# Kernel tuning notes

Hardware: AMD Instinct MI355X
Metric: run time of the kernel (lower is better)

## Reference

```python
import jax, jax.numpy as jnp
import numpy as np
from functools import partial

B, F, H, G, S = 8192, 16, 128, 4, 20  # batch, features, hidden, goals, SUBSTEPS
A_IZH, B_IZH, C_IZH, D_IZH = 0.02, 0.2, -65.0, 8.0  # Izhikevich 'RS' params
RATE_DECAY = 0.9
GAMMA, LR = 0.95, 1e-3


def izh_step(v, u, rate, I):
    """One Izhikevich substep (dt=1): returns new (v, u, rate, spike)."""
    v_new = v + (0.04 * v * v + 5.0 * v + 140.0 - u + I)
    u_new = u + A_IZH * (B_IZH * v - u)
    spike = (v_new >= 30.0).astype(v.dtype)
    v_new = jnp.where(spike > 0, C_IZH, v_new)
    u_new = u_new + spike * D_IZH
    rate_new = RATE_DECAY * rate + (1.0 - RATE_DECAY) * spike
    return v_new, u_new, rate_new, spike


def build_features(energy, threat, food_visible, goal, cls_probs, DA_, NA_):
    # [B,16] = [4 scalars | one-hot goal (4) | cls_probs (5) | DA | NA | hunger]
    base = jnp.stack([energy / 100.0, threat, food_visible, 1.0 - energy / 100.0], axis=-1)
    onehot = jax.nn.one_hot(goal, G, dtype=base.dtype)
    tail = jnp.stack([DA_, NA_, jnp.maximum(0.0, 0.5 - energy / 100.0)], axis=-1)
    return jnp.concatenate([base, onehot, cls_probs, tail], axis=-1)


def setup_inputs() -> dict:
    key = jax.random.key(0)
    ks = jax.random.split(key, 16)
    energy = jax.random.uniform(ks[0], (B,)) * 100.0
    threat = jax.random.uniform(ks[1], (B,))
    food_visible = jax.random.uniform(ks[2], (B,))
    goal = jax.random.randint(ks[3], (B,), 0, G)
    prev_goal = jax.random.randint(ks[4], (B,), 0, G)
    DA_ = jax.random.uniform(ks[5], (B,))
    NA_ = jax.random.uniform(ks[6], (B,))
    reward = jax.random.normal(ks[7], (B,)) * 0.5
    cls_probs = jax.nn.softmax(jax.random.normal(ks[8], (B, 5)), axis=-1)
    a_in = 0.5 * np.sqrt(6.0 / (F + H))   # xavier_uniform gain 0.5
    a_out = 0.3 * np.sqrt(6.0 / (H + G))  # xavier_uniform gain 0.3
    W_in_w = jax.random.uniform(ks[9], (B, H, F), minval=-a_in, maxval=a_in)
    W_in_b = jax.random.uniform(ks[10], (B, H), minval=-1.0, maxval=1.0) / np.sqrt(F)
    W_out_w = jax.random.uniform(ks[11], (B, G, H), minval=-a_out, maxval=a_out)
    W_out_b = jax.random.uniform(ks[12], (B, G), minval=-1.0, maxval=1.0) / np.sqrt(H)
    hv = jnp.full((B, H), -65.0)
    hu = B_IZH * hv
    hrate = jnp.zeros((B, H))
    vv = jnp.full((B, G), -65.0)
    vu = B_IZH * vv
    vrate = jnp.zeros((B, G))
    elig_in = jnp.zeros((B, H, F))
    elig_out = jnp.zeros((B, G, H))
    prev_values = jnp.zeros((B, G))
    prev_features = jax.random.uniform(ks[13], (B, F))
    noise = jax.random.normal(ks[14], (S, B, H))
    return dict(energy=energy, threat=threat, food_visible=food_visible, goal=goal,
                prev_goal=prev_goal, DA_=DA_, NA_=NA_, reward=reward, cls_probs=cls_probs,
                W_in_w=W_in_w, W_in_b=W_in_b, W_out_w=W_out_w, W_out_b=W_out_b,
                hv=hv, hu=hu, hrate=hrate, vv=vv, vu=vu, vrate=vrate,
                elig_in=elig_in, elig_out=elig_out, prev_values=prev_values,
                prev_features=prev_features, noise=noise)


def reference(energy, threat, food_visible, goal, prev_goal, DA_, NA_, reward, cls_probs,
              W_in_w, W_in_b, W_out_w, W_out_b, hv, hu, hrate, vv, vu, vrate,
              elig_in, elig_out, prev_values, prev_features, noise):
    features = build_features(energy, threat, food_visible, goal, cls_probs, DA_, NA_)  # [B,F]
    I_in = jnp.einsum('bhf,bf->bh', W_in_w, features) + W_in_b
    I_in = I_in * (5.0 / (jnp.mean(jnp.abs(I_in), axis=-1, keepdims=True) + 1e-8))

    def step(carry, nz):
        hv, hu, hrate, vv, vu, vrate, hsp, vsp = carry
        hv, hu, hrate, sp_h = izh_step(hv, hu, hrate, I_in + 0.3 * nz)
        I_out = jnp.einsum('bgh,bh->bg', W_out_w, hrate) + W_out_b
        I_out = I_out * (4.0 / (jnp.mean(jnp.abs(I_out), axis=-1, keepdims=True) + 1e-8))
        vv, vu, vrate, sp_v = izh_step(vv, vu, vrate, I_out)
        return (hv, hu, hrate, vv, vu, vrate, hsp + sp_h, vsp + sp_v), None

    carry0 = (hv, hu, hrate, vv, vu, vrate, jnp.zeros_like(hrate), jnp.zeros_like(vrate))
    (hv, hu, hrate, vv, vu, vrate, h_spikes, v_spikes), _ = jax.lax.scan(step, carry0, noise)

    values = jnp.einsum('bgh,bh->bg', W_out_w, hrate) + W_out_b  # [B,G]
    V_now = jnp.take_along_axis(values, goal[:, None], axis=1)[:, 0]
    V_prev = jnp.take_along_axis(prev_values, prev_goal[:, None], axis=1)[:, 0]
    td = reward + GAMMA * V_now - V_prev  # [B]

    elig_in_new = 0.9 * elig_in + hrate[:, :, None] * prev_features[:, None, :]
    elig_out_new = 0.9 * elig_out + vrate[:, :, None] * hrate[:, None, :]

    upd = (jnp.abs(td) > 1e-3)  # [B]
    scale = (LR * td * DA_)[:, None, None]
    W_in_new = jnp.where(upd[:, None, None], jnp.clip(W_in_w + scale * elig_in_new, -3.0, 3.0), W_in_w)
    W_out_new = jnp.where(upd[:, None, None], jnp.clip(W_out_w + scale * elig_out_new, -3.0, 3.0), W_out_w)

    hidden_active = jnp.mean((h_spikes > 0).astype(values.dtype), axis=-1)  # [B]
    return values, td, hidden_active, W_in_new, W_out_new, elig_in_new, elig_out_new
```

## Files before the change

### kernel.cpp

```cpp
#include <hip/hip_runtime.h>


namespace {

constexpr int F = 16;
constexpr int H = 128;
constexpr int G = 4;
constexpr int S = 20;

__device__ __forceinline__ float clip3(float x) {
    return fminf(fmaxf(x, -3.0f), 3.0f);
}

__global__ __launch_bounds__(64)
void spiking_critic_kernel(
    const float* __restrict__ energy,
    const float* __restrict__ threat,
    const float* __restrict__ food_visible,
    const int*   __restrict__ goal,
    const int*   __restrict__ prev_goal,
    const float* __restrict__ DA,
    const float* __restrict__ NA,
    const float* __restrict__ reward,
    const float* __restrict__ cls_probs,
    const float* __restrict__ W_in_w,
    const float* __restrict__ W_in_b,
    const float* __restrict__ W_out_w,
    const float* __restrict__ W_out_b,
    const float* __restrict__ hv_in,
    const float* __restrict__ hu_in,
    const float* __restrict__ hrate_in,
    const float* __restrict__ vv_in,
    const float* __restrict__ vu_in,
    const float* __restrict__ vrate_in,
    const float* __restrict__ elig_in,
    const float* __restrict__ elig_out,
    const float* __restrict__ prev_values,
    const float* __restrict__ prev_features,
    const float* __restrict__ noise,
    float* __restrict__ out_values,
    float* __restrict__ out_td,
    float* __restrict__ out_hidden,
    float* __restrict__ out_Win,
    float* __restrict__ out_Wout,
    float* __restrict__ out_ein,
    float* __restrict__ out_eout,
    int nB)
{
    const int b = blockIdx.x;
    const int t = threadIdx.x;

    __shared__ __align__(16) float w_in_lds[H * F];
    __shared__ __align__(16) float w_out_lds[G * H];
    __shared__ __align__(16) float hrate_lds[H];
    __shared__ __align__(16) float feat[F];
    __shared__ __align__(16) float pf_lds[F];

    const float4* wi4 = (const float4*)(W_in_w + (size_t)b * (H * F));
    float4* wl4 = (float4*)w_in_lds;
    #pragma unroll
    for (int k = 0; k < 8; ++k) wl4[t + 64 * k] = wi4[t + 64 * k];
    const float4* wog = (const float4*)(W_out_w + (size_t)b * (G * H));
    float4* wo4 = (float4*)w_out_lds;
    #pragma unroll
    for (int k = 0; k < 2; ++k) wo4[t + 64 * k] = wog[t + 64 * k];

    if (t < F) pf_lds[t] = prev_features[(size_t)b * F + t];

    if (t < F) {
        float e = energy[b];
        float v;
        if      (t == 0)  v = e / 100.0f;
        else if (t == 1)  v = threat[b];
        else if (t == 2)  v = food_visible[b];
        else if (t == 3)  v = 1.0f - e / 100.0f;
        else if (t < 8)   v = (goal[b] == (t - 4)) ? 1.0f : 0.0f;
        else if (t < 13)  v = cls_probs[(size_t)b * 5 + (t - 8)];
        else if (t == 13) v = DA[b];
        else if (t == 14) v = NA[b];
        else              v = fmaxf(0.0f, 0.5f - e / 100.0f);
        feat[t] = v;
    }
    __syncthreads();

    float Iraw0 = W_in_b[(size_t)b * H + t];
    float Iraw1 = W_in_b[(size_t)b * H + t + 64];
    #pragma unroll
    for (int j = 0; j < 4; ++j) {
        float4 w0 = ((const float4*)w_in_lds)[t * 4 + j];
        float4 w1 = ((const float4*)w_in_lds)[(t + 64) * 4 + j];
        float fx = feat[4 * j + 0], fy = feat[4 * j + 1];
        float fz = feat[4 * j + 2], fw = feat[4 * j + 3];
        Iraw0 += w0.x * fx + w0.y * fy + w0.z * fz + w0.w * fw;
        Iraw1 += w1.x * fx + w1.y * fy + w1.z * fz + w1.w * fw;
    }
    float a = fabsf(Iraw0) + fabsf(Iraw1);
    #pragma unroll
    for (int m = 32; m >= 1; m >>= 1) a += __shfl_xor(a, m, 64);
    float inorm = 5.0f / (a * (1.0f / 128.0f) + 1e-8f);
    float Iin0 = Iraw0 * inorm;
    float Iin1 = Iraw1 * inorm;

    float wc0[G], wc1[G], wob[G];
    #pragma unroll
    for (int g = 0; g < G; ++g) {
        wc0[g] = w_out_lds[g * H + t];
        wc1[g] = w_out_lds[g * H + t + 64];
        wob[g] = W_out_b[(size_t)b * G + g];
    }

    float hv0 = hv_in[(size_t)b * H + t],      hv1 = hv_in[(size_t)b * H + t + 64];
    float hu0 = hu_in[(size_t)b * H + t],      hu1 = hu_in[(size_t)b * H + t + 64];
    float hr0 = hrate_in[(size_t)b * H + t],   hr1 = hrate_in[(size_t)b * H + t + 64];
    float vv[G], vu[G], vr[G];
    #pragma unroll
    for (int g = 0; g < G; ++g) {
        vv[g] = vv_in[(size_t)b * G + g];
        vu[g] = vu_in[(size_t)b * G + g];
        vr[g] = vrate_in[(size_t)b * G + g];
    }

    float nz0[S], nz1[S];
    #pragma unroll
    for (int s = 0; s < S; ++s) {
        nz0[s] = noise[((size_t)s * nB + b) * H + t];
        nz1[s] = noise[((size_t)s * nB + b) * H + t + 64];
    }

    float hsp0 = 0.0f, hsp1 = 0.0f;
    float vals[G] = {0.f, 0.f, 0.f, 0.f};

    #pragma unroll
    for (int s = 0; s < S; ++s) {
        {
            float I  = Iin0 + 0.3f * nz0[s];
            float vn = hv0 + (0.04f * hv0 * hv0 + 5.0f * hv0 + 140.0f - hu0 + I);
            float un = hu0 + 0.02f * (0.2f * hv0 - hu0);
            float sp = (vn >= 30.0f) ? 1.0f : 0.0f;
            hv0 = (sp > 0.0f) ? -65.0f : vn;
            hu0 = un + sp * 8.0f;
            hr0 = 0.9f * hr0 + 0.1f * sp;
            hsp0 += sp;
        }
        {
            float I  = Iin1 + 0.3f * nz1[s];
            float vn = hv1 + (0.04f * hv1 * hv1 + 5.0f * hv1 + 140.0f - hu1 + I);
            float un = hu1 + 0.02f * (0.2f * hv1 - hu1);
            float sp = (vn >= 30.0f) ? 1.0f : 0.0f;
            hv1 = (sp > 0.0f) ? -65.0f : vn;
            hu1 = un + sp * 8.0f;
            hr1 = 0.9f * hr1 + 0.1f * sp;
            hsp1 += sp;
        }

        float p0 = wc0[0] * hr0 + wc1[0] * hr1;
        float p1 = wc0[1] * hr0 + wc1[1] * hr1;
        float p2 = wc0[2] * hr0 + wc1[2] * hr1;
        float p3 = wc0[3] * hr0 + wc1[3] * hr1;
        #pragma unroll
        for (int m = 32; m >= 1; m >>= 1) {
            p0 += __shfl_xor(p0, m, 64);
            p1 += __shfl_xor(p1, m, 64);
            p2 += __shfl_xor(p2, m, 64);
            p3 += __shfl_xor(p3, m, 64);
        }
        vals[0] = p0 + wob[0];
        vals[1] = p1 + wob[1];
        vals[2] = p2 + wob[2];
        vals[3] = p3 + wob[3];

        float m4 = 0.25f * (fabsf(vals[0]) + fabsf(vals[1])
                          + fabsf(vals[2]) + fabsf(vals[3]));
        float onorm = 4.0f / (m4 + 1e-8f);
        #pragma unroll
        for (int g = 0; g < G; ++g) {
            float Io = vals[g] * onorm;
            float vn = vv[g] + (0.04f * vv[g] * vv[g] + 5.0f * vv[g] + 140.0f - vu[g] + Io);
            float un = vu[g] + 0.02f * (0.2f * vv[g] - vu[g]);
            float sp = (vn >= 30.0f) ? 1.0f : 0.0f;
            vv[g] = (sp > 0.0f) ? -65.0f : vn;
            vu[g] = un + sp * 8.0f;
            vr[g] = 0.9f * vr[g] + 0.1f * sp;
        }
    }

    hrate_lds[t] = hr0;
    hrate_lds[t + 64] = hr1;
    __syncthreads();

    if (t < G) {
        float v = (t == 0) ? vals[0] : (t == 1) ? vals[1] : (t == 2) ? vals[2] : vals[3];
        out_values[(size_t)b * G + t] = v;
    }

    unsigned long long mb0 = __ballot(hsp0 > 0.0f);
    unsigned long long mb1 = __ballot(hsp1 > 0.0f);
    float hidden = (float)(__popcll(mb0) + __popcll(mb1)) * (1.0f / 128.0f);

    int gl = goal[b];
    float Vnow  = (gl == 0) ? vals[0] : (gl == 1) ? vals[1] : (gl == 2) ? vals[2] : vals[3];
    float Vprev = prev_values[(size_t)b * G + prev_goal[b]];
    float td = reward[b] + 0.95f * Vnow - Vprev;
    if (t == 0) {
        out_td[b]     = td;
        out_hidden[b] = hidden;
    }

    const float scale = 1e-3f * td * DA[b];
    const bool  upd   = fabsf(td) > 1e-3f;

    {
        const float4* ei4 = (const float4*)(elig_in + (size_t)b * (H * F));
        float4* oW = (float4*)(out_Win + (size_t)b * (H * F));
        float4* oE = (float4*)(out_ein + (size_t)b * (H * F));
        float4 pf = ((const float4*)pf_lds)[t & 3];
        #pragma unroll
        for (int k = 0; k < 8; ++k) {
            int q = t + 64 * k;
            float4 e  = ei4[q];
            float  hrv = hrate_lds[q >> 2];
            float4 en;
            en.x = 0.9f * e.x + hrv * pf.x;
            en.y = 0.9f * e.y + hrv * pf.y;
            en.z = 0.9f * e.z + hrv * pf.z;
            en.w = 0.9f * e.w + hrv * pf.w;
            oE[q] = en;
            float4 w = wl4[q];
            float4 wn;
            if (upd) {
                wn.x = clip3(w.x + scale * en.x);
                wn.y = clip3(w.y + scale * en.y);
                wn.z = clip3(w.z + scale * en.z);
                wn.w = clip3(w.w + scale * en.w);
            } else {
                wn = w;
            }
            oW[q] = wn;
        }
    }

    {
        const float4* eo4 = (const float4*)(elig_out + (size_t)b * (G * H));
        float4* oW = (float4*)(out_Wout + (size_t)b * (G * H));
        float4* oE = (float4*)(out_eout + (size_t)b * (G * H));
        #pragma unroll
        for (int k = 0; k < 2; ++k) {
            int q  = t + 64 * k;
            int gg = q >> 5;
            float vrv = (gg == 0) ? vr[0] : (gg == 1) ? vr[1] : (gg == 2) ? vr[2] : vr[3];
            float4 hq = ((const float4*)hrate_lds)[q & 31];
            float4 e  = eo4[q];
            float4 en;
            en.x = 0.9f * e.x + vrv * hq.x;
            en.y = 0.9f * e.y + vrv * hq.y;
            en.z = 0.9f * e.z + vrv * hq.z;
            en.w = 0.9f * e.w + vrv * hq.w;
            oE[q] = en;
            float4 w = ((const float4*)w_out_lds)[q];
            float4 wn;
            if (upd) {
                wn.x = clip3(w.x + scale * en.x);
                wn.y = clip3(w.y + scale * en.y);
                wn.z = clip3(w.z + scale * en.z);
                wn.w = clip3(w.w + scale * en.w);
            } else {
                wn = w;
            }
            oW[q] = wn;
        }
    }
}

}

extern "C" void kernel_launch(void* const* d_in, const int* in_sizes, int n_in,
                              void* d_out, int out_size, void* d_ws, size_t ws_size,
                              hipStream_t stream) {
    const int nB = in_sizes[0];

    float* out        = (float*)d_out;
    float* out_values = out;
    float* out_td     = out_values + (size_t)nB * G;
    float* out_hidden = out_td + nB;
    float* out_Win    = out_hidden + nB;
    float* out_Wout   = out_Win + (size_t)nB * H * F;
    float* out_ein    = out_Wout + (size_t)nB * G * H;
    float* out_eout   = out_ein + (size_t)nB * H * F;

    spiking_critic_kernel<<<dim3(nB), dim3(64), 0, stream>>>(
        (const float*)d_in[0],  (const float*)d_in[1],  (const float*)d_in[2],
        (const int*)  d_in[3],  (const int*)  d_in[4],
        (const float*)d_in[5],  (const float*)d_in[6],  (const float*)d_in[7],
        (const float*)d_in[8],  (const float*)d_in[9],  (const float*)d_in[10],
        (const float*)d_in[11], (const float*)d_in[12], (const float*)d_in[13],
        (const float*)d_in[14], (const float*)d_in[15], (const float*)d_in[16],
        (const float*)d_in[17], (const float*)d_in[18], (const float*)d_in[19],
        (const float*)d_in[20], (const float*)d_in[21], (const float*)d_in[22],
        (const float*)d_in[23],
        out_values, out_td, out_hidden, out_Win, out_Wout, out_ein, out_eout,
        nB);
}
```

Measured before the change: 412.5 us.

## Drop LDS staging, pack four batches per block, stream noise and use nontemporal stores

Removes all shared memory. The input-projection matvec now runs straight from global float4 loads, with a quad shuffle reduction and a permuted hidden-unit mapping. Hidden rates are exchanged through wave shuffles instead of LDS. Each 256-thread block now handles four batch rows, one wave each, with launch bounds raised for occupancy. The 20-entry noise register arrays become a two-deep prefetch ring. Outputs are written with nontemporal stores and weights are re-read from global rather than cached. All of this aims to cut LDS use, syncthreads and register pressure so more waves can hide memory latency, at the cost of re-reading the weights and doing extra shuffle work.

```diff
diff --git a/kernel.cpp b/kernel.cpp
--- a/kernel.cpp
+++ b/kernel.cpp
@@ -8,11 +8,26 @@
 constexpr int G = 4;
 constexpr int S = 20;
 
+typedef float vfloat4 __attribute__((ext_vector_type(4)));
+
 __device__ __forceinline__ float clip3(float x) {
     return fminf(fmaxf(x, -3.0f), 3.0f);
 }
 
-__global__ __launch_bounds__(64)
+__device__ __forceinline__ void nt_store4(float4 v, float4* p) {
+    vfloat4 x = {v.x, v.y, v.z, v.w};
+    __builtin_nontemporal_store(x, (vfloat4*)p);
+}
+
+__device__ __forceinline__ float hrate_at(int h, float hr0, float hr1) {
+    int m   = h >> 4;
+    int src = ((h & 15) << 2) | (m >> 1);
+    float a = __shfl(hr0, src, 64);
+    float b = __shfl(hr1, src, 64);
+    return (m & 1) ? b : a;
+}
+
+__global__ __launch_bounds__(256, 7)
 void spiking_critic_kernel(
     const float* __restrict__ energy,
     const float* __restrict__ threat,
@@ -47,93 +62,100 @@
     float* __restrict__ out_eout,
     int nB)
 {
-    const int b = blockIdx.x;
-    const int t = threadIdx.x;
-
-    __shared__ __align__(16) float w_in_lds[H * F];
-    __shared__ __align__(16) float w_out_lds[G * H];
-    __shared__ __align__(16) float hrate_lds[H];
-    __shared__ __align__(16) float feat[F];
-    __shared__ __align__(16) float pf_lds[F];
+    const int t = threadIdx.x & 63;
+    int b = blockIdx.x * 4 + (threadIdx.x >> 6);
+    b = __builtin_amdgcn_readfirstlane(b);
+    if (b >= nB) return;
+
+    const int j = t & 3;
+
+    const float e_b   = energy[b];
+    const float thr_b = threat[b];
+    const float fv_b  = food_visible[b];
+    const int   gl_b  = goal[b];
+    const float da_b  = DA[b];
+    const float na_b  = NA[b];
+    const float c0 = cls_probs[(size_t)b * 5 + 0];
+    const float c1 = cls_probs[(size_t)b * 5 + 1];
+    const float c2 = cls_probs[(size_t)b * 5 + 2];
+    const float c3 = cls_probs[(size_t)b * 5 + 3];
+    const float c4 = cls_probs[(size_t)b * 5 + 4];
+    const float en100 = e_b / 100.0f;
+
+    const float g0 = (gl_b == 0) ? 1.0f : 0.0f;
+    const float g1 = (gl_b == 1) ? 1.0f : 0.0f;
+    const float g2 = (gl_b == 2) ? 1.0f : 0.0f;
+    const float g3 = (gl_b == 3) ? 1.0f : 0.0f;
+    const float hunger = fmaxf(0.0f, 0.5f - en100);
+
+    const bool j1 = (j & 1) != 0;
+    const bool j2 = (j & 2) != 0;
+    float fx = j2 ? (j1 ? c4     : c0) : (j1 ? g0 : en100);
+    float fy = j2 ? (j1 ? da_b   : c1) : (j1 ? g1 : thr_b);
+    float fz = j2 ? (j1 ? na_b   : c2) : (j1 ? g2 : fv_b);
+    float fw = j2 ? (j1 ? hunger : c3) : (j1 ? g3 : 1.0f - en100);
 
     const float4* wi4 = (const float4*)(W_in_w + (size_t)b * (H * F));
-    float4* wl4 = (float4*)w_in_lds;
-    #pragma unroll
-    for (int k = 0; k < 8; ++k) wl4[t + 64 * k] = wi4[t + 64 * k];
-    const float4* wog = (const float4*)(W_out_w + (size_t)b * (G * H));
-    float4* wo4 = (float4*)w_out_lds;
-    #pragma unroll
-    for (int k = 0; k < 2; ++k) wo4[t + 64 * k] = wog[t + 64 * k];
-
-    if (t < F) pf_lds[t] = prev_features[(size_t)b * F + t];
-
-    if (t < F) {
-        float e = energy[b];
-        float v;
-        if      (t == 0)  v = e / 100.0f;
-        else if (t == 1)  v = threat[b];
-        else if (t == 2)  v = food_visible[b];
-        else if (t == 3)  v = 1.0f - e / 100.0f;
-        else if (t < 8)   v = (goal[b] == (t - 4)) ? 1.0f : 0.0f;
-        else if (t < 13)  v = cls_probs[(size_t)b * 5 + (t - 8)];
-        else if (t == 13) v = DA[b];
-        else if (t == 14) v = NA[b];
-        else              v = fmaxf(0.0f, 0.5f - e / 100.0f);
-        feat[t] = v;
-    }
-    __syncthreads();
-
-    float Iraw0 = W_in_b[(size_t)b * H + t];
-    float Iraw1 = W_in_b[(size_t)b * H + t + 64];
-    #pragma unroll
-    for (int j = 0; j < 4; ++j) {
-        float4 w0 = ((const float4*)w_in_lds)[t * 4 + j];
-        float4 w1 = ((const float4*)w_in_lds)[(t + 64) * 4 + j];
-        float fx = feat[4 * j + 0], fy = feat[4 * j + 1];
-        float fz = feat[4 * j + 2], fw = feat[4 * j + 3];
-        Iraw0 += w0.x * fx + w0.y * fy + w0.z * fz + w0.w * fw;
-        Iraw1 += w1.x * fx + w1.y * fy + w1.z * fz + w1.w * fw;
-    }
+    float p[8];
+    #pragma unroll
+    for (int k = 0; k < 8; ++k) {
+        float4 w = wi4[t + 64 * k];
+        p[k] = w.x * fx + w.y * fy + w.z * fz + w.w * fw;
+    }
+    #pragma unroll
+    for (int k = 0; k < 8; ++k) {
+        p[k] += __shfl_xor(p[k], 1, 64);
+        p[k] += __shfl_xor(p[k], 2, 64);
+        p[k] += W_in_b[(size_t)b * H + (t >> 2) + 16 * k];
+    }
+    const int h0 = (t >> 2) + 32 * j;
+    const int h1 = h0 + 16;
+    float Ir0a = j1 ? p[2] : p[0], Ir0b = j1 ? p[6] : p[4];
+    float Iraw0 = j2 ? Ir0b : Ir0a;
+    float Ir1a = j1 ? p[3] : p[1], Ir1b = j1 ? p[7] : p[5];
+    float Iraw1 = j2 ? Ir1b : Ir1a;
+
     float a = fabsf(Iraw0) + fabsf(Iraw1);
     #pragma unroll
     for (int m = 32; m >= 1; m >>= 1) a += __shfl_xor(a, m, 64);
-    float inorm = 5.0f / (a * (1.0f / 128.0f) + 1e-8f);
-    float Iin0 = Iraw0 * inorm;
-    float Iin1 = Iraw1 * inorm;
-
-    float wc0[G], wc1[G], wob[G];
+    const float inorm = 5.0f / (a * (1.0f / 128.0f) + 1e-8f);
+    const float Iin0 = Iraw0 * inorm;
+    const float Iin1 = Iraw1 * inorm;
+
+    float wc0[G], wc1[G], wob[G], vv[G], vu[G], vr[G];
     #pragma unroll
     for (int g = 0; g < G; ++g) {
-        wc0[g] = w_out_lds[g * H + t];
-        wc1[g] = w_out_lds[g * H + t + 64];
+        wc0[g] = W_out_w[(size_t)b * (G * H) + g * H + h0];
+        wc1[g] = W_out_w[(size_t)b * (G * H) + g * H + h1];
         wob[g] = W_out_b[(size_t)b * G + g];
-    }
-
-    float hv0 = hv_in[(size_t)b * H + t],      hv1 = hv_in[(size_t)b * H + t + 64];
-    float hu0 = hu_in[(size_t)b * H + t],      hu1 = hu_in[(size_t)b * H + t + 64];
-    float hr0 = hrate_in[(size_t)b * H + t],   hr1 = hrate_in[(size_t)b * H + t + 64];
-    float vv[G], vu[G], vr[G];
-    #pragma unroll
-    for (int g = 0; g < G; ++g) {
-        vv[g] = vv_in[(size_t)b * G + g];
-        vu[g] = vu_in[(size_t)b * G + g];
-        vr[g] = vrate_in[(size_t)b * G + g];
-    }
-
-    float nz0[S], nz1[S];
-    #pragma unroll
-    for (int s = 0; s < S; ++s) {
-        nz0[s] = noise[((size_t)s * nB + b) * H + t];
-        nz1[s] = noise[((size_t)s * nB + b) * H + t + 64];
-    }
+        vv[g]  = vv_in[(size_t)b * G + g];
+        vu[g]  = vu_in[(size_t)b * G + g];
+        vr[g]  = vrate_in[(size_t)b * G + g];
+    }
+
+    float hv0 = hv_in[(size_t)b * H + h0], hv1 = hv_in[(size_t)b * H + h1];
+    float hu0 = hu_in[(size_t)b * H + h0], hu1 = hu_in[(size_t)b * H + h1];
+    float hr0 = hrate_in[(size_t)b * H + h0], hr1 = hrate_in[(size_t)b * H + h1];
+
+    float nb0[2], nb1[2];
+    nb0[0] = noise[((size_t)0 * nB + b) * H + h0];
+    nb1[0] = noise[((size_t)0 * nB + b) * H + h1];
+    nb0[1] = noise[((size_t)1 * nB + b) * H + h0];
+    nb1[1] = noise[((size_t)1 * nB + b) * H + h1];
 
     float hsp0 = 0.0f, hsp1 = 0.0f;
     float vals[G] = {0.f, 0.f, 0.f, 0.f};
 
     #pragma unroll
     for (int s = 0; s < S; ++s) {
+        const float n0 = nb0[s & 1];
+        const float n1 = nb1[s & 1];
+        if (s + 2 < S) {
+            nb0[s & 1] = noise[((size_t)(s + 2) * nB + b) * H + h0];
+            nb1[s & 1] = noise[((size_t)(s + 2) * nB + b) * H + h1];
+        }
         {
-            float I  = Iin0 + 0.3f * nz0[s];
+            float I  = Iin0 + 0.3f * n0;
             float vn = hv0 + (0.04f * hv0 * hv0 + 5.0f * hv0 + 140.0f - hu0 + I);
             float un = hu0 + 0.02f * (0.2f * hv0 - hu0);
             float sp = (vn >= 30.0f) ? 1.0f : 0.0f;
@@ -143,7 +165,7 @@
             hsp0 += sp;
         }
         {
-            float I  = Iin1 + 0.3f * nz1[s];
+            float I  = Iin1 + 0.3f * n1;
             float vn = hv1 + (0.04f * hv1 * hv1 + 5.0f * hv1 + 140.0f - hu1 + I);
             float un = hu1 + 0.02f * (0.2f * hv1 - hu1);
             float sp = (vn >= 30.0f) ? 1.0f : 0.0f;
@@ -184,21 +206,16 @@
         }
     }
 
-    hrate_lds[t] = hr0;
-    hrate_lds[t + 64] = hr1;
-    __syncthreads();
-
     if (t < G) {
         float v = (t == 0) ? vals[0] : (t == 1) ? vals[1] : (t == 2) ? vals[2] : vals[3];
         out_values[(size_t)b * G + t] = v;
     }
-
     unsigned long long mb0 = __ballot(hsp0 > 0.0f);
     unsigned long long mb1 = __ballot(hsp1 > 0.0f);
     float hidden = (float)(__popcll(mb0) + __popcll(mb1)) * (1.0f / 128.0f);
 
-    int gl = goal[b];
-    float Vnow  = (gl == 0) ? vals[0] : (gl == 1) ? vals[1] : (gl == 2) ? vals[2] : vals[3];
+    float Vnow  = (gl_b == 0) ? vals[0] : (gl_b == 1) ? vals[1]
+                : (gl_b == 2) ? vals[2] : vals[3];
     float Vprev = prev_values[(size_t)b * G + prev_goal[b]];
     float td = reward[b] + 0.95f * Vnow - Vprev;
     if (t == 0) {
@@ -206,26 +223,34 @@
         out_hidden[b] = hidden;
     }
 
-    const float scale = 1e-3f * td * DA[b];
+    const float scale = 1e-3f * td * da_b;
     const bool  upd   = fabsf(td) > 1e-3f;
+
+    float hrk[8];
+    #pragma unroll
+    for (int jj = 0; jj < 4; ++jj) {
+        int src = (t & ~3) + jj;
+        hrk[2 * jj]     = __shfl(hr0, src, 64);
+        hrk[2 * jj + 1] = __shfl(hr1, src, 64);
+    }
 
     {
         const float4* ei4 = (const float4*)(elig_in + (size_t)b * (H * F));
         float4* oW = (float4*)(out_Win + (size_t)b * (H * F));
         float4* oE = (float4*)(out_ein + (size_t)b * (H * F));
-        float4 pf = ((const float4*)pf_lds)[t & 3];
+        float4 pf = ((const float4*)(prev_features + (size_t)b * F))[j];
         #pragma unroll
         for (int k = 0; k < 8; ++k) {
             int q = t + 64 * k;
-            float4 e  = ei4[q];
-            float  hrv = hrate_lds[q >> 2];
+            float4 e = ei4[q];
+            float4 w = wi4[q];
+            float  hrv = hrk[k];
             float4 en;
             en.x = 0.9f * e.x + hrv * pf.x;
             en.y = 0.9f * e.y + hrv * pf.y;
             en.z = 0.9f * e.z + hrv * pf.z;
             en.w = 0.9f * e.w + hrv * pf.w;
-            oE[q] = en;
-            float4 w = wl4[q];
+            nt_store4(en, &oE[q]);
             float4 wn;
             if (upd) {
                 wn.x = clip3(w.x + scale * en.x);
@@ -235,28 +260,34 @@
             } else {
                 wn = w;
             }
-            oW[q] = wn;
+            nt_store4(wn, &oW[q]);
         }
     }
 
     {
         const float4* eo4 = (const float4*)(elig_out + (size_t)b * (G * H));
+        const float4* wo4 = (const float4*)(W_out_w + (size_t)b * (G * H));
         float4* oW = (float4*)(out_Wout + (size_t)b * (G * H));
         float4* oE = (float4*)(out_eout + (size_t)b * (G * H));
         #pragma unroll
         for (int k = 0; k < 2; ++k) {
-            int q  = t + 64 * k;
-            int gg = q >> 5;
-            float vrv = (gg == 0) ? vr[0] : (gg == 1) ? vr[1] : (gg == 2) ? vr[2] : vr[3];
-            float4 hq = ((const float4*)hrate_lds)[q & 31];
-            float4 e  = eo4[q];
+            int q = t + 64 * k;
+            int c = q & 31;
+            float4 e = eo4[q];
+            float4 w = wo4[q];
+            float vrv = (k == 0) ? ((t < 32) ? vr[0] : vr[1])
+                                 : ((t < 32) ? vr[2] : vr[3]);
+            float4 hq;
+            hq.x = hrate_at(4 * c + 0, hr0, hr1);
+            hq.y = hrate_at(4 * c + 1, hr0, hr1);
+            hq.z = hrate_at(4 * c + 2, hr0, hr1);
+            hq.w = hrate_at(4 * c + 3, hr0, hr1);
             float4 en;
             en.x = 0.9f * e.x + vrv * hq.x;
             en.y = 0.9f * e.y + vrv * hq.y;
             en.z = 0.9f * e.z + vrv * hq.z;
             en.w = 0.9f * e.w + vrv * hq.w;
-            oE[q] = en;
-            float4 w = ((const float4*)w_out_lds)[q];
+            nt_store4(en, &oE[q]);
             float4 wn;
             if (upd) {
                 wn.x = clip3(w.x + scale * en.x);
@@ -266,7 +297,7 @@
             } else {
                 wn = w;
             }
-            oW[q] = wn;
+            nt_store4(wn, &oW[q]);
         }
     }
 }
@@ -287,7 +318,8 @@
     float* out_ein    = out_Wout + (size_t)nB * G * H;
     float* out_eout   = out_ein + (size_t)nB * H * F;
 
-    spiking_critic_kernel<<<dim3(nB), dim3(64), 0, stream>>>(
+    const int nBlocks = (nB + 3) / 4;
+    spiking_critic_kernel<<<dim3(nBlocks), dim3(256), 0, stream>>>(
         (const float*)d_in[0],  (const float*)d_in[1],  (const float*)d_in[2],
         (const int*)  d_in[3],  (const int*)  d_in[4],
         (const float*)d_in[5],  (const float*)d_in[6],  (const float*)d_in[7],
```

Result: slower. 657.6 us (+59.4%).
